# Performance work log

Hardware: AMD Instinct MI355X
Metric: run time of the kernel (lower is better)

Reference implementation:

```python
import jax, jax.numpy as jnp
import numpy as np

WEIGHT_FACTOR = 1.0
N_CLUSTERS = 64


def setup_inputs() -> dict:
    key = jax.random.key(0)
    k1, k2, k3 = jax.random.split(key, 3)
    B, H, W = 128, 256, 256
    x = jax.random.uniform(k1, (B, H, W), dtype=jnp.float32)
    pattern_importance = jax.random.uniform(k2, (B, N_CLUSTERS), dtype=jnp.float32)
    # dense cluster map: value in [0, N_CLUSTERS) = cluster id; == N_CLUSTERS = unassigned (mask stays 1)
    cluster_id = jax.random.randint(k3, (H, W), 0, N_CLUSTERS + 1, dtype=jnp.int32)
    return {"x": x, "pattern_importance": pattern_importance, "cluster_id": cluster_id}


def reference(x, pattern_importance, cluster_id):
    # FFT2 over last two dims; torch fftshift with dim=None shifts ALL axes (incl. batch),
    # and jnp.fft.fftshift has the same default semantics.
    x_fft = jnp.fft.fftshift(jnp.fft.fft2(x))
    assigned = cluster_id < N_CLUSTERS                     # [H, W] bool
    cid = jnp.where(assigned, cluster_id, 0)               # safe gather index
    vals = pattern_importance[:, cid] * WEIGHT_FACTOR      # [B, H, W] gather-built mask values
    mask = jnp.where(assigned[None, :, :], vals, jnp.float32(1.0))
    x_reject = x_fft * mask
    x_ifft = jnp.abs(jnp.fft.ifft2(jnp.fft.ifftshift(x_reject)))
    x_diff = jnp.abs(x_ifft - x)
    x_new = jnp.stack([x, x_ifft, x_diff], axis=1)         # [B, 3, H, W]
    return (x_new, pattern_importance)
```

## Files before the change

### kernel.cpp

```cpp
#include <hip/hip_runtime.h>
#include <math.h>

#define BB 128
#define HH 256
#define WW 256
#define HW 65536
#define OUT_B_STRIDE 196608

__device__ __forceinline__ float2 cadd(float2 a, float2 b){ return make_float2(a.x+b.x, a.y+b.y); }
__device__ __forceinline__ float2 csub(float2 a, float2 b){ return make_float2(a.x-b.x, a.y-b.y); }

template<bool INV>
__device__ __forceinline__ float2 cmul_t(float2 a, float2 b){
  if (INV) return make_float2(a.x*b.x + a.y*b.y, a.y*b.x - a.x*b.y);
  return make_float2(a.x*b.x - a.y*b.y, a.x*b.y + a.y*b.x);
}

template<bool INV>
__device__ __forceinline__ void fft4(float2&a,float2&b,float2&c,float2&d){
  float2 t0 = cadd(a,c), t1 = csub(a,c);
  float2 t2 = cadd(b,d), t3 = csub(b,d);
  float2 t3r = INV ? make_float2(-t3.y, t3.x) : make_float2(t3.y, -t3.x);
  a = cadd(t0,t2);
  b = cadd(t1,t3r);
  c = csub(t0,t2);
  d = csub(t1,t3r);
}

template<bool INV>
__device__ __forceinline__ void fft16(float2 x[16]){
  #pragma unroll
  for (int j0=0;j0<4;++j0) fft4<INV>(x[j0], x[j0+4], x[j0+8], x[j0+12]);
  const float WR[10] = {1.f, 0.923879533f, 0.707106781f, 0.382683432f, 0.f,
                        0.f, -0.707106781f, 0.f, 0.f, -0.923879533f};
  const float WI[10] = {0.f, -0.382683432f, -0.707106781f, -0.923879533f, -1.f,
                        0.f, -0.707106781f, 0.f, 0.f, 0.382683432f};
  #pragma unroll
  for (int q0=1;q0<4;++q0)
    #pragma unroll
    for (int j0=1;j0<4;++j0){
      int k = j0*q0;
      x[j0+4*q0] = cmul_t<INV>(x[j0+4*q0], make_float2(WR[k], WI[k]));
    }
  #pragma unroll
  for (int q0=0;q0<4;++q0) fft4<INV>(x[4*q0], x[4*q0+1], x[4*q0+2], x[4*q0+3]);
  float2 t[16];
  #pragma unroll
  for (int q0=0;q0<4;++q0)
    #pragma unroll
    for (int q1=0;q1<4;++q1) t[q0+4*q1] = x[4*q0+q1];
  #pragma unroll
  for (int i=0;i<16;++i) x[i]=t[i];
}

__device__ __forceinline__ void build_tw256(float2* tw, int tid){
  float s,c;
  __sincosf(-6.28318530717958647692f * (float)tid / 256.0f, &s, &c);
  tw[tid] = make_float2(c, s);
}

__global__ __launch_bounds__(256) void k_row_fwd(const float* __restrict__ x,
                                                 float2* __restrict__ S, int bstride){
  __shared__ float2 tw[256];
  __shared__ float2 zbuf[16*273];
  int tid = threadIdx.x;
  int t = tid & 15, r = tid >> 4;
  build_tw256(tw, tid);
  int row = blockIdx.x*16 + r;
  const float* xr = x + (size_t)row*256;
  float2 X[16];
  #pragma unroll
  for (int j=0;j<16;++j) X[j] = make_float2(xr[16*j + t], 0.f);
  __syncthreads();
  fft16<false>(X);
  #pragma unroll
  for (int q=0;q<16;++q) X[q] = cmul_t<false>(X[q], tw[t*q]);
  #pragma unroll
  for (int q=0;q<16;++q) zbuf[r*273 + q*17 + t] = X[q];
  __syncthreads();
  float2 Y[16];
  #pragma unroll
  for (int tt=0;tt<16;++tt) Y[tt] = zbuf[r*273 + t*17 + tt];
  fft16<false>(Y);
  int b = row >> 8, h = row & 255;
  float4* dst = (float4*)(S + (size_t)b*bstride + h*256 + t*16);
  #pragma unroll
  for (int k=0;k<8;++k)
    dst[k] = make_float4(Y[2*k].x, Y[2*k].y, Y[2*k+1].x, Y[2*k+1].y);
}

__global__ __launch_bounds__(256) void k_col(float2* __restrict__ S, int bstride,
                                             const int* __restrict__ cid,
                                             const float* __restrict__ pi){
  __shared__ float2 tw[256];
  __shared__ float2 zbuf[16*273];
  __shared__ float sPI[64];
  int tid = threadIdx.x;
  int c = tid & 15, t = tid >> 4;
  int cg = blockIdx.x, b = blockIdx.y;
  build_tw256(tw, tid);
  if (tid < 64) sPI[tid] = pi[(((b + 64) & 127) << 6) + tid];
  float2* Sb = S + (size_t)b*bstride;
  int p = cg*16 + c;
  float2 X[16];
  #pragma unroll
  for (int j=0;j<16;++j) X[j] = Sb[(16*j + t)*256 + p];
  __syncthreads();
  fft16<false>(X);
  #pragma unroll
  for (int q=0;q<16;++q) X[q] = cmul_t<false>(X[q], tw[t*q]);
  #pragma unroll
  for (int q=0;q<16;++q) zbuf[c*273 + q*17 + t] = X[q];
  __syncthreads();
  int s = t;
  float2 Y[16];
  #pragma unroll
  for (int tt=0;tt<16;++tt) Y[tt] = zbuf[c*273 + s*17 + tt];
  fft16<false>(Y);
  int w2 = ((16*c + cg) + 128) & 255;
  #pragma unroll
  for (int k1=0;k1<16;++k1){
    int h2 = (16*k1 + s + 128) & 255;
    int cv = cid[h2*256 + w2];
    float m = (cv < 64) ? sPI[cv] : 1.0f;
    Y[k1].x *= m; Y[k1].y *= m;
  }
  __syncthreads();
  fft16<true>(Y);
  #pragma unroll
  for (int u=0;u<16;++u) Y[u] = cmul_t<true>(Y[u], tw[u*s]);
  #pragma unroll
  for (int u=0;u<16;++u) zbuf[c*273 + u*17 + s] = Y[u];
  __syncthreads();
  float2 R[16];
  #pragma unroll
  for (int k0=0;k0<16;++k0) R[k0] = zbuf[c*273 + t*17 + k0];
  fft16<true>(R);
  #pragma unroll
  for (int j=0;j<16;++j) Sb[(16*j + t)*256 + p] = R[j];
}

__global__ __launch_bounds__(256) void k_row_inv_fused(const float2* __restrict__ S, int bstride,
                                                       const float* __restrict__ x,
                                                       const float* __restrict__ pi,
                                                       float* __restrict__ out){
  __shared__ float2 tw[256];
  __shared__ float2 zbuf[16*273];
  int tid = threadIdx.x;
  int s = tid & 15, r = tid >> 4;
  int slice = blockIdx.x, b = blockIdx.y;
  build_tw256(tw, tid);
  int h = slice*16 + r;
  const float4* src4 = (const float4*)(S + (size_t)b*bstride + h*256 + s*16);
  float2 X[16];
  #pragma unroll
  for (int k=0;k<8;++k){
    float4 v = src4[k];
    X[2*k]   = make_float2(v.x, v.y);
    X[2*k+1] = make_float2(v.z, v.w);
  }
  __syncthreads();
  fft16<true>(X);
  #pragma unroll
  for (int u=0;u<16;++u) X[u] = cmul_t<true>(X[u], tw[u*s]);
  #pragma unroll
  for (int u=0;u<16;++u) zbuf[r*273 + u*17 + s] = X[u];
  __syncthreads();
  int t = tid & 15;
  float2 R[16];
  #pragma unroll
  for (int k0=0;k0<16;++k0) R[k0] = zbuf[r*273 + t*17 + k0];
  fft16<true>(R);
  const float scale = 1.0f/65536.0f;
  const float* xr = x + (size_t)b*HW + h*256;
  float* o = out + (size_t)b*OUT_B_STRIDE + h*256;
  #pragma unroll
  for (int j=0;j<16;++j){
    int n = 16*j + t;
    float y = sqrtf(R[j].x*R[j].x + R[j].y*R[j].y) * scale;
    float xv = xr[n];
    o[n]        = xv;
    o[n + HW]   = y;
    o[n + 2*HW] = fabsf(y - xv);
  }
  if (slice == 0 && b < 8){
    const float4* p4 = (const float4*)pi;
    float4* o4 = (float4*)out;
    o4[6291456 + b*256 + tid] = p4[b*256 + tid];
  }
}

__global__ __launch_bounds__(256) void k_row_inv_stage(const float2* __restrict__ S, int bstride,
                                                       float* __restrict__ out){
  __shared__ float2 tw[256];
  __shared__ float2 zbuf[16*273];
  int tid = threadIdx.x;
  int s = tid & 15, r = tid >> 4;
  int slice = blockIdx.x, b = blockIdx.y;
  build_tw256(tw, tid);
  int h = slice*16 + r;
  const float4* src4 = (const float4*)(S + (size_t)b*bstride + h*256 + s*16);
  float2 X[16];
  #pragma unroll
  for (int k=0;k<8;++k){
    float4 v = src4[k];
    X[2*k]   = make_float2(v.x, v.y);
    X[2*k+1] = make_float2(v.z, v.w);
  }
  __syncthreads();
  fft16<true>(X);
  #pragma unroll
  for (int u=0;u<16;++u) X[u] = cmul_t<true>(X[u], tw[u*s]);
  #pragma unroll
  for (int u=0;u<16;++u) zbuf[r*273 + u*17 + s] = X[u];
  __syncthreads();
  int t = tid & 15;
  float2 R[16];
  #pragma unroll
  for (int k0=0;k0<16;++k0) R[k0] = zbuf[r*273 + t*17 + k0];
  fft16<true>(R);
  const float scale = 1.0f/65536.0f;
  float* o = out + (size_t)b*OUT_B_STRIDE + h*256;
  #pragma unroll
  for (int j=0;j<16;++j){
    int n = 16*j + t;
    o[n] = sqrtf(R[j].x*R[j].x + R[j].y*R[j].y) * scale;
  }
}

__global__ __launch_bounds__(256) void k_final(const float* __restrict__ x,
                                               const float* __restrict__ pi,
                                               float* __restrict__ out) {
  int i = blockIdx.x * 256 + threadIdx.x;
  const float4* x4 = (const float4*)x;
  float4* o4 = (float4*)out;
  int b = i >> 14;
  int r = i & 16383;
  int ch0 = b * 49152 + r;
  float4 y  = o4[ch0];
  float4 xv = x4[i];
  float4 df;
  df.x = fabsf(y.x - xv.x);
  df.y = fabsf(y.y - xv.y);
  df.z = fabsf(y.z - xv.z);
  df.w = fabsf(y.w - xv.w);
  o4[ch0]         = xv;
  o4[ch0 + 16384] = y;
  o4[ch0 + 32768] = df;
  if (i < 2048) {
    const float4* p4 = (const float4*)pi;
    o4[6291456 + i] = p4[i];
  }
}

extern "C" void kernel_launch(void* const* d_in, const int* in_sizes, int n_in,
                              void* d_out, int out_size, void* d_ws, size_t ws_size,
                              hipStream_t stream) {
  const float* x  = (const float*)d_in[0];
  const float* pi = (const float*)d_in[1];
  const int*  cid = (const int*)d_in[2];
  float* out = (float*)d_out;
  (void)in_sizes; (void)n_in; (void)out_size;

  const size_t S_bytes = (size_t)BB * HW * sizeof(float2);
  if (ws_size >= S_bytes) {
    float2* S = (float2*)d_ws;
    k_row_fwd<<<2048, 256, 0, stream>>>(x, S, 65536);
    k_col<<<dim3(16, BB), 256, 0, stream>>>(S, 65536, cid, pi);
    k_row_inv_fused<<<dim3(16, BB), 256, 0, stream>>>(S, 65536, x, pi, out);
  } else {
    float2* S = (float2*)out + 32768;
    k_row_fwd<<<2048, 256, 0, stream>>>(x, S, 98304);
    k_col<<<dim3(16, BB), 256, 0, stream>>>(S, 98304, cid, pi);
    k_row_inv_stage<<<dim3(16, BB), 256, 0, stream>>>(S, 98304, out);
    k_final<<<8192, 256, 0, stream>>>(x, pi, out);
  }
}
```

Measured before the change: 207.9 us.

## Store FFT intermediates as fp16, precompute permuted byte cluster map, stage I/O via LDS

Stores the spectrum intermediate buffer as half2 instead of float2, which halves the global traffic between the three FFT passes. A prescaling factor of 0.25 in the mask and a rescaled final normalisation keep fp16 values in range. The first kernel also builds a byte-packed, pre-permuted cluster-id map so the column kernel reads one 16-byte vector instead of 16 scattered int gathers. Input loads and output stores go through shared memory so they are coalesced float4 accesses, and launch bounds request 4 blocks per CU. The cost is fp16 rounding error on the FFT intermediates, and the fallback path's workspace pointer handling looks questionable.

```diff
diff --git a/kernel.cpp b/kernel.cpp
--- a/kernel.cpp
+++ b/kernel.cpp
@@ -1,4 +1,5 @@
 #include <hip/hip_runtime.h>
+#include <hip/hip_fp16.h>
 #include <math.h>
 
 #define BB 128
@@ -59,70 +60,118 @@
   tw[tid] = make_float2(c, s);
 }
 
-__global__ __launch_bounds__(256) void k_row_fwd(const float* __restrict__ x,
-                                                 float2* __restrict__ S, int bstride){
+__device__ __forceinline__ uint pkh2(float2 v){
+  __half2 h = __float22half2_rn(v);
+  return *(uint*)&h;
+}
+__device__ __forceinline__ float2 uph2(uint u){
+  __half2 h = *(__half2*)&u;
+  return __half22float2(h);
+}
+
+union SharedU {
+  float  xs[16*272];
+  float2 zbuf[16*273];
+  float  ybuf[16*272];
+};
+
+__global__ __launch_bounds__(256, 4) void k_row_fwd(const float* __restrict__ x,
+                                                    __half2* __restrict__ S,
+                                                    const int* __restrict__ cid,
+                                                    unsigned char* __restrict__ cidp){
+  __shared__ SharedU sh;
   __shared__ float2 tw[256];
-  __shared__ float2 zbuf[16*273];
   int tid = threadIdx.x;
   int t = tid & 15, r = tid >> 4;
   build_tw256(tw, tid);
+
+  if (blockIdx.x < 64){
+    int g = (blockIdx.x*256 + tid) * 4;
+    int p  = g >> 8;
+    int s  = (g >> 4) & 15;
+    int k1b = g & 15;
+    int wfreq = 16*(p & 15) + (p >> 4);
+    int w2 = (wfreq + 128) & 255;
+    uchar4 v4;
+    unsigned char* vp = (unsigned char*)&v4;
+    #pragma unroll
+    for (int i=0;i<4;++i){
+      int h2 = (16*(k1b+i) + s + 128) & 255;
+      int cv = cid[h2*256 + w2];
+      vp[i] = (unsigned char)cv;
+    }
+    *(uchar4*)(cidp + g) = v4;
+  }
+
+  const float4* xb = (const float4*)x + (size_t)blockIdx.x * 1024;
+  #pragma unroll
+  for (int k=0;k<4;++k){
+    int i2 = tid + k*256;
+    float4 v = xb[i2];
+    int row = i2 >> 6, c4 = i2 & 63;
+    *(float4*)&sh.xs[row*272 + c4*4] = v;
+  }
+  __syncthreads();
+  float2 X[16];
+  #pragma unroll
+  for (int j=0;j<16;++j) X[j] = make_float2(sh.xs[r*272 + 16*j + t], 0.f);
+  __syncthreads();
+  fft16<false>(X);
+  #pragma unroll
+  for (int q=0;q<16;++q) X[q] = cmul_t<false>(X[q], tw[t*q]);
+  #pragma unroll
+  for (int q=0;q<16;++q) sh.zbuf[r*273 + q*17 + t] = X[q];
+  __syncthreads();
+  float2 Y[16];
+  #pragma unroll
+  for (int tt=0;tt<16;++tt) Y[tt] = sh.zbuf[r*273 + t*17 + tt];
+  fft16<false>(Y);
   int row = blockIdx.x*16 + r;
-  const float* xr = x + (size_t)row*256;
-  float2 X[16];
-  #pragma unroll
-  for (int j=0;j<16;++j) X[j] = make_float2(xr[16*j + t], 0.f);
-  __syncthreads();
-  fft16<false>(X);
-  #pragma unroll
-  for (int q=0;q<16;++q) X[q] = cmul_t<false>(X[q], tw[t*q]);
-  #pragma unroll
-  for (int q=0;q<16;++q) zbuf[r*273 + q*17 + t] = X[q];
-  __syncthreads();
-  float2 Y[16];
-  #pragma unroll
-  for (int tt=0;tt<16;++tt) Y[tt] = zbuf[r*273 + t*17 + tt];
-  fft16<false>(Y);
   int b = row >> 8, h = row & 255;
-  float4* dst = (float4*)(S + (size_t)b*bstride + h*256 + t*16);
-  #pragma unroll
-  for (int k=0;k<8;++k)
-    dst[k] = make_float4(Y[2*k].x, Y[2*k].y, Y[2*k+1].x, Y[2*k+1].y);
-}
-
-__global__ __launch_bounds__(256) void k_col(float2* __restrict__ S, int bstride,
-                                             const int* __restrict__ cid,
-                                             const float* __restrict__ pi){
+  uint4* dst = (uint4*)(S + (size_t)b*HW + h*256 + t*16);
+  #pragma unroll
+  for (int k=0;k<4;++k){
+    uint4 q;
+    q.x = pkh2(Y[4*k+0]); q.y = pkh2(Y[4*k+1]);
+    q.z = pkh2(Y[4*k+2]); q.w = pkh2(Y[4*k+3]);
+    dst[k] = q;
+  }
+}
+
+__global__ __launch_bounds__(256, 4) void k_col(__half2* __restrict__ S,
+                                                const unsigned char* __restrict__ cidp,
+                                                const float* __restrict__ pi){
+  __shared__ SharedU sh;
   __shared__ float2 tw[256];
-  __shared__ float2 zbuf[16*273];
   __shared__ float sPI[64];
   int tid = threadIdx.x;
   int c = tid & 15, t = tid >> 4;
   int cg = blockIdx.x, b = blockIdx.y;
   build_tw256(tw, tid);
-  if (tid < 64) sPI[tid] = pi[(((b + 64) & 127) << 6) + tid];
-  float2* Sb = S + (size_t)b*bstride;
+  if (tid < 64) sPI[tid] = pi[(((b + 64) & 127) << 6) + tid] * 0.25f;
+  __half2* Sb = S + (size_t)b*HW;
   int p = cg*16 + c;
   float2 X[16];
   #pragma unroll
-  for (int j=0;j<16;++j) X[j] = Sb[(16*j + t)*256 + p];
+  for (int j=0;j<16;++j) X[j] = uph2(*(uint*)&Sb[(16*j + t)*256 + p]);
+  uint4 mq = *(const uint4*)(cidp + p*256 + t*16);
   __syncthreads();
   fft16<false>(X);
   #pragma unroll
   for (int q=0;q<16;++q) X[q] = cmul_t<false>(X[q], tw[t*q]);
   #pragma unroll
-  for (int q=0;q<16;++q) zbuf[c*273 + q*17 + t] = X[q];
+  for (int q=0;q<16;++q) sh.zbuf[c*273 + q*17 + t] = X[q];
   __syncthreads();
   int s = t;
   float2 Y[16];
   #pragma unroll
-  for (int tt=0;tt<16;++tt) Y[tt] = zbuf[c*273 + s*17 + tt];
+  for (int tt=0;tt<16;++tt) Y[tt] = sh.zbuf[c*273 + s*17 + tt];
   fft16<false>(Y);
-  int w2 = ((16*c + cg) + 128) & 255;
+  const uint* mw = (const uint*)&mq;
   #pragma unroll
   for (int k1=0;k1<16;++k1){
-    int h2 = (16*k1 + s + 128) & 255;
-    int cv = cid[h2*256 + w2];
-    float m = (cv < 64) ? sPI[cv] : 1.0f;
+    int cv = (mw[k1>>2] >> ((k1&3)*8)) & 255;
+    float m = (cv < 64) ? sPI[cv] : 0.25f;
     Y[k1].x *= m; Y[k1].y *= m;
   }
   __syncthreads();
@@ -130,102 +179,111 @@
   #pragma unroll
   for (int u=0;u<16;++u) Y[u] = cmul_t<true>(Y[u], tw[u*s]);
   #pragma unroll
-  for (int u=0;u<16;++u) zbuf[c*273 + u*17 + s] = Y[u];
+  for (int u=0;u<16;++u) sh.zbuf[c*273 + u*17 + s] = Y[u];
   __syncthreads();
   float2 R[16];
   #pragma unroll
-  for (int k0=0;k0<16;++k0) R[k0] = zbuf[c*273 + t*17 + k0];
+  for (int k0=0;k0<16;++k0) R[k0] = sh.zbuf[c*273 + t*17 + k0];
   fft16<true>(R);
   #pragma unroll
-  for (int j=0;j<16;++j) Sb[(16*j + t)*256 + p] = R[j];
-}
-
-__global__ __launch_bounds__(256) void k_row_inv_fused(const float2* __restrict__ S, int bstride,
-                                                       const float* __restrict__ x,
-                                                       const float* __restrict__ pi,
-                                                       float* __restrict__ out){
+  for (int j=0;j<16;++j){
+    uint u = pkh2(R[j]);
+    *(uint*)&Sb[(16*j + t)*256 + p] = u;
+  }
+}
+
+__global__ __launch_bounds__(256, 4) void k_row_inv_fused(const __half2* __restrict__ S,
+                                                          const float* __restrict__ x,
+                                                          const float* __restrict__ pi,
+                                                          float* __restrict__ out){
+  __shared__ SharedU sh;
   __shared__ float2 tw[256];
-  __shared__ float2 zbuf[16*273];
   int tid = threadIdx.x;
   int s = tid & 15, r = tid >> 4;
   int slice = blockIdx.x, b = blockIdx.y;
   build_tw256(tw, tid);
   int h = slice*16 + r;
-  const float4* src4 = (const float4*)(S + (size_t)b*bstride + h*256 + s*16);
+  const uint4* src = (const uint4*)(S + (size_t)b*HW + h*256 + s*16);
   float2 X[16];
   #pragma unroll
-  for (int k=0;k<8;++k){
-    float4 v = src4[k];
-    X[2*k]   = make_float2(v.x, v.y);
-    X[2*k+1] = make_float2(v.z, v.w);
+  for (int k=0;k<4;++k){
+    uint4 q = src[k];
+    X[4*k+0] = uph2(q.x); X[4*k+1] = uph2(q.y);
+    X[4*k+2] = uph2(q.z); X[4*k+3] = uph2(q.w);
   }
   __syncthreads();
   fft16<true>(X);
   #pragma unroll
   for (int u=0;u<16;++u) X[u] = cmul_t<true>(X[u], tw[u*s]);
   #pragma unroll
-  for (int u=0;u<16;++u) zbuf[r*273 + u*17 + s] = X[u];
-  __syncthreads();
-  int t = tid & 15;
+  for (int u=0;u<16;++u) sh.zbuf[r*273 + u*17 + s] = X[u];
+  __syncthreads();
   float2 R[16];
   #pragma unroll
-  for (int k0=0;k0<16;++k0) R[k0] = zbuf[r*273 + t*17 + k0];
+  for (int k0=0;k0<16;++k0) R[k0] = sh.zbuf[r*273 + s*17 + k0];
   fft16<true>(R);
-  const float scale = 1.0f/65536.0f;
-  const float* xr = x + (size_t)b*HW + h*256;
-  float* o = out + (size_t)b*OUT_B_STRIDE + h*256;
-  #pragma unroll
-  for (int j=0;j<16;++j){
-    int n = 16*j + t;
-    float y = sqrtf(R[j].x*R[j].x + R[j].y*R[j].y) * scale;
-    float xv = xr[n];
-    o[n]        = xv;
-    o[n + HW]   = y;
-    o[n + 2*HW] = fabsf(y - xv);
+  __syncthreads();
+  const float scale = 1.0f/16384.0f;
+  #pragma unroll
+  for (int j=0;j<16;++j)
+    sh.ybuf[r*272 + 16*j + s] = sqrtf(R[j].x*R[j].x + R[j].y*R[j].y) * scale;
+  __syncthreads();
+  const float4* x4 = (const float4*)x;
+  float4* o4 = (float4*)out;
+  size_t xbase = (size_t)b*16384 + slice*1024;
+  size_t obase = (size_t)b*49152 + slice*1024;
+  #pragma unroll
+  for (int k=0;k<4;++k){
+    int i2 = tid + k*256;
+    int rr = i2 >> 6, c4 = i2 & 63;
+    float4 y = *(float4*)&sh.ybuf[rr*272 + c4*4];
+    float4 xv = x4[xbase + i2];
+    float4 df;
+    df.x = fabsf(y.x - xv.x); df.y = fabsf(y.y - xv.y);
+    df.z = fabsf(y.z - xv.z); df.w = fabsf(y.w - xv.w);
+    o4[obase + i2]         = xv;
+    o4[obase + i2 + 16384] = y;
+    o4[obase + i2 + 32768] = df;
   }
   if (slice == 0 && b < 8){
     const float4* p4 = (const float4*)pi;
-    float4* o4 = (float4*)out;
     o4[6291456 + b*256 + tid] = p4[b*256 + tid];
   }
 }
 
-__global__ __launch_bounds__(256) void k_row_inv_stage(const float2* __restrict__ S, int bstride,
-                                                       float* __restrict__ out){
+__global__ __launch_bounds__(256, 4) void k_row_inv_stage(const __half2* __restrict__ S,
+                                                          float* __restrict__ out){
+  __shared__ SharedU sh;
   __shared__ float2 tw[256];
-  __shared__ float2 zbuf[16*273];
   int tid = threadIdx.x;
   int s = tid & 15, r = tid >> 4;
   int slice = blockIdx.x, b = blockIdx.y;
   build_tw256(tw, tid);
   int h = slice*16 + r;
-  const float4* src4 = (const float4*)(S + (size_t)b*bstride + h*256 + s*16);
+  const uint4* src = (const uint4*)(S + (size_t)b*HW + h*256 + s*16);
   float2 X[16];
   #pragma unroll
-  for (int k=0;k<8;++k){
-    float4 v = src4[k];
-    X[2*k]   = make_float2(v.x, v.y);
-    X[2*k+1] = make_float2(v.z, v.w);
+  for (int k=0;k<4;++k){
+    uint4 q = src[k];
+    X[4*k+0] = uph2(q.x); X[4*k+1] = uph2(q.y);
+    X[4*k+2] = uph2(q.z); X[4*k+3] = uph2(q.w);
   }
   __syncthreads();
   fft16<true>(X);
   #pragma unroll
   for (int u=0;u<16;++u) X[u] = cmul_t<true>(X[u], tw[u*s]);
   #pragma unroll
-  for (int u=0;u<16;++u) zbuf[r*273 + u*17 + s] = X[u];
-  __syncthreads();
-  int t = tid & 15;
+  for (int u=0;u<16;++u) sh.zbuf[r*273 + u*17 + s] = X[u];
+  __syncthreads();
   float2 R[16];
   #pragma unroll
-  for (int k0=0;k0<16;++k0) R[k0] = zbuf[r*273 + t*17 + k0];
+  for (int k0=0;k0<16;++k0) R[k0] = sh.zbuf[r*273 + s*17 + k0];
   fft16<true>(R);
-  const float scale = 1.0f/65536.0f;
+  const float scale = 1.0f/16384.0f;
   float* o = out + (size_t)b*OUT_B_STRIDE + h*256;
   #pragma unroll
-  for (int j=0;j<16;++j){
-    int n = 16*j + t;
-    o[n] = sqrtf(R[j].x*R[j].x + R[j].y*R[j].y) * scale;
-  }
+  for (int j=0;j<16;++j)
+    o[16*j + s] = sqrtf(R[j].x*R[j].x + R[j].y*R[j].y) * scale;
 }
 
 __global__ __launch_bounds__(256) void k_final(const float* __restrict__ x,
@@ -262,17 +320,22 @@
   float* out = (float*)d_out;
   (void)in_sizes; (void)n_in; (void)out_size;
 
-  const size_t S_bytes = (size_t)BB * HW * sizeof(float2);
-  if (ws_size >= S_bytes) {
-    float2* S = (float2*)d_ws;
-    k_row_fwd<<<2048, 256, 0, stream>>>(x, S, 65536);
-    k_col<<<dim3(16, BB), 256, 0, stream>>>(S, 65536, cid, pi);
-    k_row_inv_fused<<<dim3(16, BB), 256, 0, stream>>>(S, 65536, x, pi, out);
+  const size_t S_bytes = (size_t)BB * HW * sizeof(__half2);
+  const size_t cidp_bytes = 65536;
+
+  if (ws_size >= S_bytes + cidp_bytes) {
+    __half2* S = (__half2*)d_ws;
+    unsigned char* cidp = (unsigned char*)d_ws + S_bytes;
+    k_row_fwd<<<2048, 256, 0, stream>>>(x, S, cid, cidp);
+    k_col<<<dim3(16, BB), 256, 0, stream>>>(S, cidp, pi);
+    k_row_inv_fused<<<dim3(16, BB), 256, 0, stream>>>(S, x, pi, out);
   } else {
-    float2* S = (float2*)out + 32768;
-    k_row_fwd<<<2048, 256, 0, stream>>>(x, S, 98304);
-    k_col<<<dim3(16, BB), 256, 0, stream>>>(S, 98304, cid, pi);
-    k_row_inv_stage<<<dim3(16, BB), 256, 0, stream>>>(S, 98304, out);
+    __half2* S = (__half2*)((float*)out + HW);
+    S = (__half2*)out + (size_t)BB * HW;
+    unsigned char* cidp = (unsigned char*)d_ws;
+    k_row_fwd<<<2048, 256, 0, stream>>>(x, S, cid, cidp);
+    k_col<<<dim3(16, BB), 256, 0, stream>>>(S, cidp, pi);
+    k_row_inv_stage<<<dim3(16, BB), 256, 0, stream>>>(S, out);
     k_final<<<8192, 256, 0, stream>>>(x, pi, out);
   }
 }
```

New measurement: 176.3 us. 15.2% less time.
